# Kernel optimization log

Measured on AMD Instinct MI355X. Metric: run time of the kernel, lower is better.

The kernel has to match this reference:

```python
import jax, jax.numpy as jnp
import numpy as np

B, S, D, E, TOP_K = 16, 2048, 240, 8, 2


def setup_inputs() -> dict:
    key = jax.random.key(0)
    k1, k2, k3 = jax.random.split(key, 3)
    scale = 1.0 / np.sqrt(D)
    return {
        "x": jax.random.normal(k1, (B, S, D), dtype=jnp.float32),
        "gate_w": jax.random.normal(k2, (E, D), dtype=jnp.float32) * scale,
        "gate_b": jnp.zeros((E,), dtype=jnp.float32),
        "expert_w": jax.random.normal(k3, (E, D, D), dtype=jnp.float32) * scale,
        "expert_b": jnp.zeros((E, D), dtype=jnp.float32),
    }


def reference(x, gate_w, gate_b, expert_w, expert_b):
    # Gating: softmax over experts, pick top-k, renormalize.
    logits = jnp.einsum("bsd,ed->bse", x, gate_w) + gate_b          # [B,S,E]
    gate_weights = jax.nn.softmax(logits, axis=-1)
    topk_w, topk_i = jax.lax.top_k(gate_weights, TOP_K)             # [B,S,K]
    topk_w = topk_w / jnp.sum(topk_w, axis=-1, keepdims=True)
    # Scatter renormalized top-k weights back to dense per-expert weights.
    onehot = jax.nn.one_hot(topk_i, E, dtype=x.dtype)               # [B,S,K,E]
    w_full = jnp.sum(topk_w[..., None] * onehot, axis=-2)           # [B,S,E]
    # Expert linears (torch Linear: y = x @ W^T + b), combined by gate weight.
    h = jnp.einsum("bsd,eod->bseo", x, expert_w) + expert_b         # [B,S,E,D]
    return jnp.einsum("bseo,bse->bso", h, w_full)                   # [B,S,D]
```

## Files before the change

### kernel.cpp

```cpp
#include <hip/hip_runtime.h>
#include <hip/hip_bf16.h>

#define TOKENS 32768
#define Dm 240
#define DP 256
#define NE 8
#define BK 32
#define NCHUNK 8
#define TILE_M 64
#define NB 64
#define CSTR 16

typedef __bf16 bf16x8 __attribute__((ext_vector_type(8)));
typedef float  f32x4  __attribute__((ext_vector_type(4)));

__device__ __forceinline__ float b2f(unsigned short u) {
    union { unsigned int i; float f; } v; v.i = ((unsigned int)u) << 16; return v.f;
}
__device__ __forceinline__ float b2f_lo(unsigned u) {
    union { unsigned int i; float f; } v; v.i = u << 16; return v.f;
}
__device__ __forceinline__ float b2f_hi(unsigned u) {
    union { unsigned int i; float f; } v; v.i = u & 0xFFFF0000u; return v.f;
}
__device__ __forceinline__ unsigned short f2b(float f) {
    unsigned int i = __builtin_bit_cast(unsigned int, f);
    unsigned int r = (i + 0x7FFFu + ((i >> 16) & 1u)) >> 16;
    return (unsigned short)r;
}
__device__ __forceinline__ unsigned short f2h(float f) {
    _Float16 h = (_Float16)f;
    union { _Float16 h; unsigned short u; } v; v.h = h; return v.u;
}
__device__ __forceinline__ float h2f(unsigned short u) {
    union { _Float16 h; unsigned short u; } v; v.u = u; return (float)v.h;
}
__device__ __forceinline__ uint4 pack8(float4 a, float4 b) {
    union { unsigned short u[8]; uint4 v; } r;
    r.u[0] = f2b(a.x); r.u[1] = f2b(a.y); r.u[2] = f2b(a.z); r.u[3] = f2b(a.w);
    r.u[4] = f2b(b.x); r.u[5] = f2b(b.y); r.u[6] = f2b(b.z); r.u[7] = f2b(b.w);
    return r.v;
}

__device__ __forceinline__ void gload_lds16(const void* g, void* l) {
    __builtin_amdgcn_global_load_lds(
        (const __attribute__((address_space(1))) void*)g,
        (__attribute__((address_space(3))) void*)l,
        16, 0, 0);
}

__device__ __forceinline__ bool block_detect_f32(const unsigned short* x,
                                                 int tid, int* dh) {
    if (tid == 0) *dh = 0;
    __syncthreads();
    if (tid < 256) {
        uint4 q = *(const uint4*)&x[tid * 8];
        unsigned w[4] = {q.x, q.y, q.z, q.w};
        int hits = 0;
        #pragma unroll
        for (int i = 0; i < 4; i++) {
            if ((((w[i] & 0xFFFFu) >> 7) & 0xFFu) >= 0xC0u) hits++;
            if ((((w[i] >> 16)      >> 7) & 0xFFu) >= 0xC0u) hits++;
        }
        if (hits) atomicAdd(dh, hits);
    }
    __syncthreads();
    return *dh > 8;
}

__global__ __launch_bounds__(256) void gatewconv_kernel(
    const void* __restrict__ xv, const void* __restrict__ gwv,
    const void* __restrict__ gbv,
    const void* __restrict__ ewv, const void* __restrict__ ebv,
    int* __restrict__ flag, int* __restrict__ cnt,
    unsigned* __restrict__ rt, unsigned short* __restrict__ xpad,
    unsigned short* __restrict__ wpad, float* __restrict__ ebpad)
{
    __shared__ float gwsF[NE * Dm];
    __shared__ int h[NB];
    __shared__ int base[NB];
    __shared__ int dh;

    int tid = threadIdx.x;
    const bool f32 = block_detect_f32((const unsigned short*)xv, tid, &dh);

    if (blockIdx.x < 256) {
        if (blockIdx.x == 0 && tid == 0) flag[0] = f32 ? 1 : 0;

        int gidx = blockIdx.x * 256 + tid;

        if (gidx < NE * DP) {
            int e = gidx >> 8, n = gidx & 255;
            float bv = 0.f;
            if (n < Dm)
                bv = f32 ? ((const float*)ebv)[e * Dm + n]
                         : b2f(((const unsigned short*)ebv)[e * Dm + n]);
            ebpad[gidx] = bv;
        }

        int n = gidx & 255;
        int s = (gidx >> 8) & 3;
        int c = (gidx >> 10) & 7;
        int e = gidx >> 13;
        int k = c * 32 + s * 8;
        uint4 v = make_uint4(0, 0, 0, 0);
        if (n < Dm && k < Dm) {
            if (f32) {
                const float* src = (const float*)ewv + ((long)e * Dm + n) * Dm + k;
                v = pack8(*(const float4*)src, *(const float4*)(src + 4));
            } else {
                v = *(const uint4*)((const unsigned short*)ewv + ((long)e * Dm + n) * Dm + k);
            }
        }
        *(uint4*)&wpad[(long)gidx * 8] = v;
        return;
    }

    int gbid = blockIdx.x - 256;
    if (tid < NB) h[tid] = 0;

    if (f32) {
        if (tid < 240) {
            const float* s = (const float*)gwv + tid * 8;
            float4 a = *(const float4*)s;
            float4 b4 = *(const float4*)(s + 4);
            float* d = &gwsF[tid * 8];
            *(float4*)d = a; *(float4*)(d + 4) = b4;
        }
    } else {
        if (tid < 240) {
            unsigned short* gb16 = (unsigned short*)gwsF;
            *(uint4*)&gb16[tid * 8] =
                *(const uint4*)((const unsigned short*)gwv + tid * 8);
        }
    }
    __syncthreads();

    int grp = tid >> 3;
    int j   = tid & 7;
    int t   = gbid * 32 + grp;

    float acc[NE] = {0.f, 0.f, 0.f, 0.f, 0.f, 0.f, 0.f, 0.f};
    unsigned short* xo = xpad + (long)t * DP;

    if (f32) {
        const float* xf = (const float*)xv + (long)t * Dm;
        #pragma unroll
        for (int i = 0; i < 4; i++) {
            int g = j + 8 * i;
            if (g < 30) {
                float4 xa = *(const float4*)&xf[g * 8];
                float4 xb = *(const float4*)&xf[g * 8 + 4];
                *(uint4*)&xo[g * 8] = pack8(xa, xb);
                #pragma unroll
                for (int e = 0; e < NE; e++) {
                    const float* gp = &gwsF[e * Dm + g * 8];
                    float4 ga = *(const float4*)gp;
                    float4 gc = *(const float4*)(gp + 4);
                    acc[e] += xa.x * ga.x + xa.y * ga.y + xa.z * ga.z + xa.w * ga.w
                            + xb.x * gc.x + xb.y * gc.y + xb.z * gc.z + xb.w * gc.w;
                }
            } else {
                *(uint4*)&xo[g * 8] = make_uint4(0, 0, 0, 0);
            }
        }
    } else {
        const unsigned short* xb = (const unsigned short*)xv + (long)t * Dm;
        const unsigned short* gb16 = (const unsigned short*)gwsF;
        #pragma unroll
        for (int i = 0; i < 4; i++) {
            int g = j + 8 * i;
            if (g < 30) {
                uint4 xq = *(const uint4*)&xb[g * 8];
                *(uint4*)&xo[g * 8] = xq;
                float x0 = b2f_lo(xq.x), x1 = b2f_hi(xq.x);
                float x2 = b2f_lo(xq.y), x3 = b2f_hi(xq.y);
                float x4 = b2f_lo(xq.z), x5 = b2f_hi(xq.z);
                float x6 = b2f_lo(xq.w), x7 = b2f_hi(xq.w);
                #pragma unroll
                for (int e = 0; e < NE; e++) {
                    uint4 gq = *(const uint4*)&gb16[e * Dm + g * 8];
                    acc[e] += x0 * b2f_lo(gq.x) + x1 * b2f_hi(gq.x)
                            + x2 * b2f_lo(gq.y) + x3 * b2f_hi(gq.y)
                            + x4 * b2f_lo(gq.z) + x5 * b2f_hi(gq.z)
                            + x6 * b2f_lo(gq.w) + x7 * b2f_hi(gq.w);
                }
            } else {
                *(uint4*)&xo[g * 8] = make_uint4(0, 0, 0, 0);
            }
        }
    }

    #pragma unroll
    for (int m = 1; m < 8; m <<= 1)
        #pragma unroll
        for (int e = 0; e < NE; e++)
            acc[e] += __shfl_xor(acc[e], m, 64);

    int bb = 0; float w0 = 0.f;
    if (j == 0) {
        #pragma unroll
        for (int e = 0; e < NE; e++)
            acc[e] += f32 ? ((const float*)gbv)[e]
                          : b2f(((const unsigned short*)gbv)[e]);
        float l0 = -1e30f; int e0 = 0;
        #pragma unroll
        for (int e = 0; e < NE; e++) if (acc[e] > l0) { l0 = acc[e]; e0 = e; }
        float l1 = -1e30f; int e1 = 0;
        #pragma unroll
        for (int e = 0; e < NE; e++) if (e != e0 && acc[e] > l1) { l1 = acc[e]; e1 = e; }
        w0 = 1.f / (1.f + __expf(l1 - l0));
        bb = e0 * 8 + e1;
        atomicAdd(&h[bb], 1);
    }
    __syncthreads();
    if (tid < NB) {
        int i = (tid + gbid) & (NB - 1);
        int c = h[i];
        if (c) base[i] = atomicAdd(&cnt[i * CSTR], c);
        h[i] = 0;
    }
    __syncthreads();
    if (j == 0) {
        int o = atomicAdd(&h[bb], 1);
        rt[bb * TOKENS + base[bb] + o] = ((unsigned)t << 16) | (unsigned)f2h(w0);
    }
}

__global__ __launch_bounds__(512, 2) void expert_kernel(
    const unsigned short* __restrict__ xp,
    const unsigned short* __restrict__ wp,
    const float* __restrict__ ebpad,
    const int* __restrict__ flag,
    const int* __restrict__ cnt, const unsigned* __restrict__ rt,
    void* __restrict__ outv)
{
    __shared__ __align__(16) unsigned short Xc[NCHUNK][4][64][8];

    int b  = blockIdx.y;
    int ne = cnt[b * CSTR];
    if (ne == 0) return;
    int ntile = (ne + 63) >> 6;
    if ((int)blockIdx.x >= ntile) return;

    const bool f32o = (*flag != 0);
    int e0 = b >> 3, e1 = b & 7;

    int tid  = threadIdx.x;
    int lane = tid & 63;
    int w    = tid >> 6;

    int frow = lane & 15;
    int slot = lane >> 4;
    const unsigned short* wb0 = wp + (long)e0 * 65536 + slot * 2048
                                   + (w * 32 + frow) * 8;
    const unsigned short* wb1 = wp + (long)e1 * 65536 + slot * 2048
                                   + (w * 32 + frow) * 8;
    int colg = lane & 15;
    int rq   = (lane >> 4) << 2;
    float b0n[2], b1n[2];
    #pragma unroll
    for (int nt = 0; nt < 2; nt++) {
        int n = w * 32 + nt * 16 + colg;
        b0n[nt] = ebpad[e0 * DP + n];
        b1n[nt] = ebpad[e1 * DP + n];
    }

    for (int t = blockIdx.x; t < ntile; t += 8) {
        int m0 = t * TILE_M;
        int rows = min(TILE_M, ne - m0);

        unsigned rvp = rt[b * TOKENS + min(m0 + lane, ne - 1)];
        int   tokL = (int)(rvp >> 16);
        float w0L  = h2f((unsigned short)(rvp & 0xFFFFu));

        const unsigned short* xbase = xp + (long)tokL * DP;
        #pragma unroll
        for (int i = 0; i < 4; i++)
            gload_lds16(xbase + w * BK + i * 8, &Xc[w][i][0][0]);
        __syncthreads();

        f32x4 acc0[4][2] = {};
        f32x4 acc1[4][2] = {};

        #pragma unroll
        for (int c = 0; c < NCHUNK; c++) {
            bf16x8 a[4], b0[2], b1[2];
            #pragma unroll
            for (int mt = 0; mt < 4; mt++)
                a[mt] = *(const bf16x8*)&Xc[c][slot][mt * 16 + frow][0];
            #pragma unroll
            for (int nt = 0; nt < 2; nt++) {
                b0[nt] = *(const bf16x8*)&wb0[c * 8192 + nt * 128];
                b1[nt] = *(const bf16x8*)&wb1[c * 8192 + nt * 128];
            }
            #pragma unroll
            for (int nt = 0; nt < 2; nt++)
                #pragma unroll
                for (int mt = 0; mt < 4; mt++) {
                    acc0[mt][nt] = __builtin_amdgcn_mfma_f32_16x16x32_bf16(
                        a[mt], b0[nt], acc0[mt][nt], 0, 0, 0);
                    acc1[mt][nt] = __builtin_amdgcn_mfma_f32_16x16x32_bf16(
                        a[mt], b1[nt], acc1[mt][nt], 0, 0, 0);
                }
        }

        #pragma unroll
        for (int mt = 0; mt < 4; mt++) {
            #pragma unroll
            for (int r = 0; r < 4; r++) {
                int m = mt * 16 + rq + r;
                int   tok = __shfl(tokL, m);
                float w0  = __shfl(w0L, m);
                float w1  = 1.f - w0;
                if (m < rows) {
                    #pragma unroll
                    for (int nt = 0; nt < 2; nt++) {
                        int n = w * 32 + nt * 16 + colg;
                        if (n < Dm) {
                            float val = (acc0[mt][nt][r] + b0n[nt]) * w0
                                      + (acc1[mt][nt][r] + b1n[nt]) * w1;
                            long idx = (long)tok * Dm + n;
                            if (f32o) ((float*)outv)[idx] = val;
                            else      ((unsigned short*)outv)[idx] = f2b(val);
                        }
                    }
                }
            }
        }

        if (t + 8 < ntile) __syncthreads();
    }
}

__global__ void detect_kernel(const unsigned short* __restrict__ x, int* flag,
                              int* __restrict__ cnt) {
    int lane = threadIdx.x;
    cnt[lane] = 0;
    int hits = 0;
    for (int i = lane; i < 2048; i += 64) {
        unsigned e = (x[i] >> 7) & 0xFFu;
        if (e >= 0xC0u) hits++;
    }
    #pragma unroll
    for (int off = 32; off >= 1; off >>= 1) hits += __shfl_xor(hits, off, 64);
    if (lane == 0) flag[0] = (hits > 8) ? 1 : 0;
}

__global__ void init_kernel(int* cnt) {
    if (threadIdx.x < 16) cnt[threadIdx.x] = 0;
}

__global__ void zero_kernel(void* outv, const int* flag, int nelem) {
    long i = (long)blockIdx.x * blockDim.x + threadIdx.x;
    long stride = (long)gridDim.x * blockDim.x;
    if (*flag) {
        float* o = (float*)outv;
        for (; i < nelem; i += stride) o[i] = 0.f;
    } else {
        unsigned* o = (unsigned*)outv;
        long n = nelem >> 1;
        for (; i < n; i += stride) o[i] = 0u;
    }
}

template<bool FP32>
__global__ __launch_bounds__(256) void gate_fb_kernel(
    const void* __restrict__ xv, const void* __restrict__ gwv,
    const void* __restrict__ gbv, const int* __restrict__ flag,
    int* __restrict__ cnt, unsigned* __restrict__ rt, int cap)
{
    if ((*flag != 0) != FP32) return;
    __shared__ unsigned rv[256];
    __shared__ int h[16];
    __shared__ int base[16];

    int tid = threadIdx.x;
    if (tid < 16) h[tid] = 0;
    int t = blockIdx.x * 256 + tid;

    float acc[NE];
    #pragma unroll
    for (int e = 0; e < NE; e++)
        acc[e] = FP32 ? ((const float*)gbv)[e]
                      : b2f(((const unsigned short*)gbv)[e]);

    if (FP32) {
        const float* xf  = (const float*)xv + (long)t * Dm;
        const float* gwf = (const float*)gwv;
        for (int k = 0; k < Dm; k += 8) {
            float4 xa = *(const float4*)&xf[k];
            float4 xb = *(const float4*)&xf[k + 4];
            #pragma unroll
            for (int e = 0; e < NE; e++) {
                float4 ga = *(const float4*)&gwf[e * Dm + k];
                float4 gb = *(const float4*)&gwf[e * Dm + k + 4];
                acc[e] += xa.x * ga.x + xa.y * ga.y + xa.z * ga.z + xa.w * ga.w
                        + xb.x * gb.x + xb.y * gb.y + xb.z * gb.z + xb.w * gb.w;
            }
        }
    } else {
        const unsigned short* xb  = (const unsigned short*)xv + (long)t * Dm;
        const unsigned short* gwb = (const unsigned short*)gwv;
        for (int k = 0; k < Dm; k += 8) {
            uint4 xq = *(const uint4*)&xb[k];
            float x0 = b2f_lo(xq.x), x1 = b2f_hi(xq.x);
            float x2 = b2f_lo(xq.y), x3 = b2f_hi(xq.y);
            float x4 = b2f_lo(xq.z), x5 = b2f_hi(xq.z);
            float x6 = b2f_lo(xq.w), x7 = b2f_hi(xq.w);
            #pragma unroll
            for (int e = 0; e < NE; e++) {
                uint4 gq = *(const uint4*)&gwb[e * Dm + k];
                acc[e] += x0 * b2f_lo(gq.x) + x1 * b2f_hi(gq.x)
                        + x2 * b2f_lo(gq.y) + x3 * b2f_hi(gq.y)
                        + x4 * b2f_lo(gq.z) + x5 * b2f_hi(gq.z)
                        + x6 * b2f_lo(gq.w) + x7 * b2f_hi(gq.w);
            }
        }
    }

    float l0 = -1e30f; int e0 = 0;
    #pragma unroll
    for (int e = 0; e < NE; e++) if (acc[e] > l0) { l0 = acc[e]; e0 = e; }
    float l1 = -1e30f; int e1 = 0;
    #pragma unroll
    for (int e = 0; e < NE; e++) if (e != e0 && acc[e] > l1) { l1 = acc[e]; e1 = e; }
    float w0 = 1.f / (1.f + __expf(l1 - l0));

    rv[tid] = ((unsigned)e1 << 20) | ((unsigned)e0 << 16) | (unsigned)f2h(w0);
    __syncthreads();

    {
        unsigned v = rv[tid];
        atomicAdd(&h[(v >> 16) & 7], 1);
        atomicAdd(&h[8 + ((v >> 20) & 7)], 1);
    }
    __syncthreads();

    if (tid < 16) {
        base[tid] = atomicAdd(&cnt[tid], h[tid]);
        h[tid] = 0;
    }
    __syncthreads();

    {
        unsigned v = rv[tid];
        int tt = blockIdx.x * 256 + tid;
        int a0 = (v >> 16) & 7;
        int a1 = (v >> 20) & 7;
        unsigned short hw0 = (unsigned short)(v & 0xFFFFu);
        int o0 = atomicAdd(&h[a0], 1);
        int p0 = base[a0] + o0;
        if (p0 < cap) rt[a0 * cap + p0] = ((unsigned)tt << 16) | hw0;
        int o1 = atomicAdd(&h[8 + a1], 1);
        int p1 = base[8 + a1] + o1;
        if (p1 < cap) rt[(8 + a1) * cap + p1] = ((unsigned)tt << 16) | (unsigned)f2h(1.f - h2f(hw0));
    }
}

template<bool FP32>
__global__ __launch_bounds__(256) void expert_fb_kernel(
    const void* __restrict__ xv, const void* __restrict__ ewv,
    const void* __restrict__ ebv, const int* __restrict__ flag,
    const int* __restrict__ cnt, const unsigned* __restrict__ rt, int cap,
    void* __restrict__ outv, int slotBase, int accumulate)
{
    if ((*flag != 0) != FP32) return;
    int e = blockIdx.y;
    int tile = blockIdx.x;
    int bucket = slotBase + e;
    int ne = min(cnt[bucket], cap);
    int m0 = tile * TILE_M;
    if (m0 >= ne) return;
    int rows = min(TILE_M, ne - m0);

    __shared__ __align__(16) unsigned short Wcf[2][256][40];
    __shared__ __align__(16) unsigned short Xcf[2][TILE_M][40];
    __shared__ int   tokS[TILE_M];
    __shared__ float twS[TILE_M];

    int tid = threadIdx.x;
    if (tid < TILE_M) {
        int i = min(m0 + tid, ne - 1);
        unsigned v = rt[bucket * cap + i];
        tokS[tid] = (int)(v >> 16);
        twS[tid]  = (tid < rows) ? h2f((unsigned short)(v & 0xFFFFu)) : 0.f;
    }
    __syncthreads();

    int srow = tid >> 2;
    int part = tid & 3;

    auto stage = [&](int c, int buf) {
        int kk = c * BK + part * 8;
        bool kvalid = (kk < Dm);
        if (FP32) {
            const float* xf = (const float*)xv;
            const float* Wf = (const float*)ewv + e * Dm * Dm;
            uint4 xq = make_uint4(0, 0, 0, 0);
            if (kvalid) {
                const float* s = &xf[(long)tokS[srow] * Dm + kk];
                xq = pack8(*(const float4*)s, *(const float4*)(s + 4));
            }
            *(uint4*)&Xcf[buf][srow][part * 8] = xq;
            #pragma unroll
            for (int it = 0; it < 4; it++) {
                int n = srow + it * 64;
                uint4 wq = make_uint4(0, 0, 0, 0);
                if (kvalid && n < Dm) {
                    const float* s = &Wf[(long)n * Dm + kk];
                    wq = pack8(*(const float4*)s, *(const float4*)(s + 4));
                }
                *(uint4*)&Wcf[buf][n][part * 8] = wq;
            }
        } else {
            const unsigned short* xb = (const unsigned short*)xv;
            const unsigned short* Wb = (const unsigned short*)ewv + e * Dm * Dm;
            uint4 xq = make_uint4(0, 0, 0, 0);
            if (kvalid) xq = *(const uint4*)&xb[(long)tokS[srow] * Dm + kk];
            *(uint4*)&Xcf[buf][srow][part * 8] = xq;
            #pragma unroll
            for (int it = 0; it < 4; it++) {
                int n = srow + it * 64;
                uint4 wq = make_uint4(0, 0, 0, 0);
                if (kvalid && n < Dm) wq = *(const uint4*)&Wb[(long)n * Dm + kk];
                *(uint4*)&Wcf[buf][n][part * 8] = wq;
            }
        }
    };

    int lane = tid & 63;
    int wv   = tid >> 6;
    int frow = lane & 15;
    int koff = (lane >> 4) * 8;

    f32x4 acc[TILE_M / 16][4] = {};

    stage(0, 0);
    __syncthreads();
    for (int c = 0; c < NCHUNK; c++) {
        int buf = c & 1;
        bf16x8 a[TILE_M / 16], b[4];
        #pragma unroll
        for (int mt = 0; mt < TILE_M / 16; mt++)
            a[mt] = *(const bf16x8*)&Xcf[buf][mt * 16 + frow][koff];
        #pragma unroll
        for (int nt = 0; nt < 4; nt++)
            b[nt] = *(const bf16x8*)&Wcf[buf][wv * 64 + nt * 16 + frow][koff];
        if (c + 1 < NCHUNK) stage(c + 1, (c + 1) & 1);
        #pragma unroll
        for (int mt = 0; mt < TILE_M / 16; mt++)
            #pragma unroll
            for (int nt = 0; nt < 4; nt++)
                acc[mt][nt] = __builtin_amdgcn_mfma_f32_16x16x32_bf16(
                    a[mt], b[nt], acc[mt][nt], 0, 0, 0);
        __syncthreads();
    }

    int colg  = lane & 15;
    int rquad = (lane >> 4) * 4;
    #pragma unroll
    for (int nt = 0; nt < 4; nt++) {
        int n = wv * 64 + nt * 16 + colg;
        if (n >= Dm) continue;
        float bnv = FP32 ? ((const float*)ebv)[e * Dm + n]
                         : b2f(((const unsigned short*)ebv)[e * Dm + n]);
        #pragma unroll
        for (int mt = 0; mt < TILE_M / 16; mt++) {
            #pragma unroll
            for (int r = 0; r < 4; r++) {
                int m = mt * 16 + rquad + r;
                if (m < rows) {
                    float val = (acc[mt][nt][r] + bnv) * twS[m];
                    long idx = (long)tokS[m] * Dm + n;
                    if (FP32) {
                        float* o = (float*)outv + idx;
                        *o = accumulate ? (*o + val) : val;
                    } else {
                        unsigned short* o = (unsigned short*)outv + idx;
                        *o = accumulate ? f2b(b2f(*o) + val) : f2b(val);
                    }
                }
            }
        }
    }
}

extern "C" void kernel_launch(void* const* d_in, const int* in_sizes, int n_in,
                              void* d_out, int out_size, void* d_ws, size_t ws_size,
                              hipStream_t stream) {
    const void* x  = d_in[0];
    const void* gw = d_in[1];
    const void* gb = d_in[2];
    const void* ew = d_in[3];
    const void* eb = d_in[4];

    char* ws = (char*)d_ws;
    int* flag = (int*)ws;
    int* cnt  = (int*)(ws + 64);

    const size_t EB_OFF = 64 + (size_t)NB * CSTR * 4;
    const size_t RT_OFF = EB_OFF + (size_t)NE * DP * 4;
    const size_t XP_OFF = RT_OFF + (size_t)NB * TOKENS * 4;
    const size_t WP_OFF = XP_OFF + (size_t)TOKENS * DP * 2;
    const size_t NEEDED = WP_OFF + (size_t)NE * NCHUNK * 8192 * 2;

    if (ws_size >= NEEDED) {
        float*          ebpad = (float*)(ws + EB_OFF);
        unsigned*       rt    = (unsigned*)(ws + RT_OFF);
        unsigned short* xpad  = (unsigned short*)(ws + XP_OFF);
        unsigned short* wpad  = (unsigned short*)(ws + WP_OFF);

        hipMemsetAsync(ws, 0, EB_OFF, stream);
        gatewconv_kernel<<<1280, 256, 0, stream>>>(
            x, gw, gb, ew, eb, flag, cnt, rt, xpad, wpad, ebpad);
        expert_kernel<<<dim3(8, NB), 512, 0, stream>>>(
            xpad, wpad, ebpad, flag, cnt, rt, d_out);
    } else {
        unsigned* rt = (unsigned*)(ws + 128);
        long capl = ((long)ws_size - 128) / (16 * sizeof(unsigned));
        if (capl > TOKENS) capl = TOKENS;
        if (capl < 64) capl = 64;
        int cap = (int)capl;
        int tiles = (cap + TILE_M - 1) / TILE_M;
        bool lossless = (cap >= TOKENS);
        int acc0 = lossless ? 0 : 1;

        detect_kernel<<<1, 64, 0, stream>>>((const unsigned short*)x, flag, cnt);
        init_kernel<<<1, 64, 0, stream>>>(cnt);
        gate_fb_kernel<false><<<TOKENS / 256, 256, 0, stream>>>(x, gw, gb, flag, cnt, rt, cap);
        gate_fb_kernel<true ><<<TOKENS / 256, 256, 0, stream>>>(x, gw, gb, flag, cnt, rt, cap);
        if (!lossless)
            zero_kernel<<<1024, 256, 0, stream>>>(d_out, flag, out_size);
        expert_fb_kernel<false><<<dim3(tiles, NE), 256, 0, stream>>>(x, ew, eb, flag, cnt, rt, cap, d_out, 0, acc0);
        expert_fb_kernel<true ><<<dim3(tiles, NE), 256, 0, stream>>>(x, ew, eb, flag, cnt, rt, cap, d_out, 0, acc0);
        expert_fb_kernel<false><<<dim3(tiles, NE), 256, 0, stream>>>(x, ew, eb, flag, cnt, rt, cap, d_out, 8, 1);
        expert_fb_kernel<true ><<<dim3(tiles, NE), 256, 0, stream>>>(x, ew, eb, flag, cnt, rt, cap, d_out, 8, 1);
    }
}
```

Before: 153.5 us.

## Write gate-kernel activations directly into per-bucket compacted rows for contiguous expert loads

The gate kernel now scatters each token's bf16 activation row into a per-expert-pair compacted buffer (capped at XCAP rows per bucket), falling back to the token-indexed padded buffer on overflow. The expert kernel then loads its X tiles from contiguous compacted rows instead of gathering by token index, removing the dependent load on the routing table before the tile loads. The grid is also transposed so bucket index is blockIdx.x, which changes block scheduling order. This costs extra workspace and makes the gate-kernel stores scattered.

Result: faster. 149.3 us (-2.7%).

```diff
diff --git a/kernel.cpp b/kernel.cpp
--- a/kernel.cpp
+++ b/kernel.cpp
@@ -10,6 +10,7 @@
 #define TILE_M 64
 #define NB 64
 #define CSTR 16
+#define XCAP 2048
 
 typedef __bf16 bf16x8 __attribute__((ext_vector_type(8)));
 typedef float  f32x4  __attribute__((ext_vector_type(4)));
@@ -73,7 +74,8 @@
     const void* __restrict__ gbv,
     const void* __restrict__ ewv, const void* __restrict__ ebv,
     int* __restrict__ flag, int* __restrict__ cnt,
-    unsigned* __restrict__ rt, unsigned short* __restrict__ xpad,
+    unsigned* __restrict__ rt, unsigned short* __restrict__ xc,
+    unsigned short* __restrict__ xpad,
     unsigned short* __restrict__ wpad, float* __restrict__ ebpad)
 {
     __shared__ float gwsF[NE * Dm];
@@ -141,7 +143,7 @@
     int t   = gbid * 32 + grp;
 
     float acc[NE] = {0.f, 0.f, 0.f, 0.f, 0.f, 0.f, 0.f, 0.f};
-    unsigned short* xo = xpad + (long)t * DP;
+    uint4 xg[4];
 
     if (f32) {
         const float* xf = (const float*)xv + (long)t * Dm;
@@ -151,7 +153,7 @@
             if (g < 30) {
                 float4 xa = *(const float4*)&xf[g * 8];
                 float4 xb = *(const float4*)&xf[g * 8 + 4];
-                *(uint4*)&xo[g * 8] = pack8(xa, xb);
+                xg[i] = pack8(xa, xb);
                 #pragma unroll
                 for (int e = 0; e < NE; e++) {
                     const float* gp = &gwsF[e * Dm + g * 8];
@@ -161,7 +163,7 @@
                             + xb.x * gc.x + xb.y * gc.y + xb.z * gc.z + xb.w * gc.w;
                 }
             } else {
-                *(uint4*)&xo[g * 8] = make_uint4(0, 0, 0, 0);
+                xg[i] = make_uint4(0, 0, 0, 0);
             }
         }
     } else {
@@ -172,7 +174,7 @@
             int g = j + 8 * i;
             if (g < 30) {
                 uint4 xq = *(const uint4*)&xb[g * 8];
-                *(uint4*)&xo[g * 8] = xq;
+                xg[i] = xq;
                 float x0 = b2f_lo(xq.x), x1 = b2f_hi(xq.x);
                 float x2 = b2f_lo(xq.y), x3 = b2f_hi(xq.y);
                 float x4 = b2f_lo(xq.z), x5 = b2f_hi(xq.z);
@@ -186,7 +188,7 @@
                             + x6 * b2f_lo(gq.w) + x7 * b2f_hi(gq.w);
                 }
             } else {
-                *(uint4*)&xo[g * 8] = make_uint4(0, 0, 0, 0);
+                xg[i] = make_uint4(0, 0, 0, 0);
             }
         }
     }
@@ -221,14 +223,27 @@
         h[i] = 0;
     }
     __syncthreads();
+
+    long row = 0;
     if (j == 0) {
         int o = atomicAdd(&h[bb], 1);
-        rt[bb * TOKENS + base[bb] + o] = ((unsigned)t << 16) | (unsigned)f2h(w0);
+        int p = base[bb] + o;
+        rt[bb * TOKENS + p] = ((unsigned)t << 16) | (unsigned)f2h(w0);
+        row = (p < XCAP) ? ((long)bb * XCAP + p) : -1L;
+    }
+    row = __shfl(row, (tid & 63) & ~7);
+    unsigned short* dst = (row >= 0) ? xc + row * DP
+                                     : xpad + (long)t * DP;
+    #pragma unroll
+    for (int i = 0; i < 4; i++) {
+        int g = j + 8 * i;
+        *(uint4*)&dst[g * 8] = xg[i];
     }
 }
 
 __global__ __launch_bounds__(512, 2) void expert_kernel(
-    const unsigned short* __restrict__ xp,
+    const unsigned short* __restrict__ xc,
+    const unsigned short* __restrict__ xpad,
     const unsigned short* __restrict__ wp,
     const float* __restrict__ ebpad,
     const int* __restrict__ flag,
@@ -237,11 +252,11 @@
 {
     __shared__ __align__(16) unsigned short Xc[NCHUNK][4][64][8];
 
-    int b  = blockIdx.y;
+    int b  = blockIdx.x;
     int ne = cnt[b * CSTR];
     if (ne == 0) return;
     int ntile = (ne + 63) >> 6;
-    if ((int)blockIdx.x >= ntile) return;
+    if ((int)blockIdx.y >= ntile) return;
 
     const bool f32o = (*flag != 0);
     int e0 = b >> 3, e1 = b & 7;
@@ -266,18 +281,30 @@
         b1n[nt] = ebpad[e1 * DP + n];
     }
 
-    for (int t = blockIdx.x; t < ntile; t += 8) {
+    for (int t = blockIdx.y; t < ntile; t += 8) {
         int m0 = t * TILE_M;
         int rows = min(TILE_M, ne - m0);
+
+        if (m0 + TILE_M <= XCAP) {
+            const unsigned short* xsrc = xc + ((long)b * XCAP + m0 + lane) * DP;
+            #pragma unroll
+            for (int i = 0; i < 4; i++)
+                gload_lds16(xsrc + w * BK + i * 8, &Xc[w][i][0][0]);
+        } else {
+            unsigned rv_ = rt[b * TOKENS + min(m0 + lane, ne - 1)];
+            long ii = m0 + lane;
+            const unsigned short* xsrc = (ii < XCAP)
+                ? xc + ((long)b * XCAP + ii) * DP
+                : xpad + (long)(rv_ >> 16) * DP;
+            #pragma unroll
+            for (int i = 0; i < 4; i++)
+                gload_lds16(xsrc + w * BK + i * 8, &Xc[w][i][0][0]);
+        }
 
         unsigned rvp = rt[b * TOKENS + min(m0 + lane, ne - 1)];
         int   tokL = (int)(rvp >> 16);
         float w0L  = h2f((unsigned short)(rvp & 0xFFFFu));
 
-        const unsigned short* xbase = xp + (long)tokL * DP;
-        #pragma unroll
-        for (int i = 0; i < 4; i++)
-            gload_lds16(xbase + w * BK + i * 8, &Xc[w][i][0][0]);
         __syncthreads();
 
         f32x4 acc0[4][2] = {};
@@ -602,20 +629,22 @@
     const size_t EB_OFF = 64 + (size_t)NB * CSTR * 4;
     const size_t RT_OFF = EB_OFF + (size_t)NE * DP * 4;
     const size_t XP_OFF = RT_OFF + (size_t)NB * TOKENS * 4;
-    const size_t WP_OFF = XP_OFF + (size_t)TOKENS * DP * 2;
+    const size_t XC_OFF = XP_OFF + (size_t)TOKENS * DP * 2;
+    const size_t WP_OFF = XC_OFF + (size_t)NB * XCAP * DP * 2;
     const size_t NEEDED = WP_OFF + (size_t)NE * NCHUNK * 8192 * 2;
 
     if (ws_size >= NEEDED) {
         float*          ebpad = (float*)(ws + EB_OFF);
         unsigned*       rt    = (unsigned*)(ws + RT_OFF);
         unsigned short* xpad  = (unsigned short*)(ws + XP_OFF);
+        unsigned short* xcb   = (unsigned short*)(ws + XC_OFF);
         unsigned short* wpad  = (unsigned short*)(ws + WP_OFF);
 
         hipMemsetAsync(ws, 0, EB_OFF, stream);
         gatewconv_kernel<<<1280, 256, 0, stream>>>(
-            x, gw, gb, ew, eb, flag, cnt, rt, xpad, wpad, ebpad);
-        expert_kernel<<<dim3(8, NB), 512, 0, stream>>>(
-            xpad, wpad, ebpad, flag, cnt, rt, d_out);
+            x, gw, gb, ew, eb, flag, cnt, rt, xcb, xpad, wpad, ebpad);
+        expert_kernel<<<dim3(NB, 8), 512, 0, stream>>>(
+            xcb, xpad, wpad, ebpad, flag, cnt, rt, d_out);
     } else {
         unsigned* rt = (unsigned*)(ws + 128);
         long capl = ((long)ws_size - 128) / (16 * sizeof(unsigned));
```
